# Optimization experiments

Measured on AMD Instinct MI355X. Metric: run time of the kernel, lower is better.

Reference implementation:

```python
import jax, jax.numpy as jnp
import numpy as np

B, N, H, M = 1, 1024, 64, 32


def _posenc(n, d):
    # sinusoidal positional encoding, matches torch PositionalEncoding (eval mode, no dropout)
    pos = jnp.arange(n, dtype=jnp.float32)[:, None]
    div = jnp.exp(jnp.arange(0, d, 2, dtype=jnp.float32) * (-np.log(10000.0) / d))
    ang = pos * div  # [n, d//2]
    pe = jnp.zeros((n, d), jnp.float32)
    pe = pe.at[:, 0::2].set(jnp.sin(ang))
    pe = pe.at[:, 1::2].set(jnp.cos(ang))
    return pe


def _egnn(x, h, m2f, w_msg, b_msg, w_pos, b_pos, w_feat, b_feat):
    # x: [B,N,3], h: [B,N,Hd], m2f: [B,N,N] float pair mask (diag zero)
    Bn, Nn, Hd = h.shape
    m2 = m2f[..., None]
    # r[b,i,j] = x[b,j] - x[b,i]  (torch: x.unsqueeze(-3) - x.unsqueeze(-2))
    r = (x[:, None, :, :] - x[:, :, None, :]) * m2  # [B,N,N,3]
    d2 = jnp.sum(r * r, axis=-1)  # [B,N,N]
    # message_mlp(cat(hi, hj, d2)): hi[b,i,j]=h[j], hj[b,i,j]=h[i]
    # split weight to avoid materializing the N x N x (2H+1) concat
    Wa, Wb, wd = w_msg[:, :Hd], w_msg[:, Hd:2 * Hd], w_msg[:, 2 * Hd]
    A = h @ Wa.T   # [B,N,M], contribution of h_j (hi slot)
    Bm = h @ Wb.T  # [B,N,M], contribution of h_i (hj slot)
    m = jax.nn.relu(A[:, None, :, :] + Bm[:, :, None, :] + d2[..., None] * wd + b_msg) * m2  # [B,N,N,M]
    mx = (m @ w_pos.T + b_pos) * r  # [B,N,N,3]
    x = x + jnp.sum(mx, axis=-2) / (Nn - 1)
    msum = jnp.sum(m, axis=-2)  # [B,N,M]
    h = jnp.concatenate([h, msum], axis=-1) @ w_feat.T + b_feat  # [B,N,Hd]
    return x, h


def setup_inputs() -> dict:
    key = jax.random.key(0)
    ks = jax.random.split(key, 16)
    def lin_w(k, o, i):
        return (jax.random.normal(k, (o, i), jnp.float32) / np.sqrt(i)).astype(jnp.float32)
    def lin_b(k, o):
        return (jax.random.normal(k, (o,), jnp.float32) * 0.02).astype(jnp.float32)
    return {
        'positions': jax.random.normal(ks[0], (B, N, 3), jnp.float32),
        'features': jax.random.normal(ks[1], (B, N, H), jnp.float32),
        'mask': jnp.ones((B, N), dtype=bool),
        'w_msg1': lin_w(ks[2], M, 2 * H + 1), 'b_msg1': lin_b(ks[3], M),
        'w_pos1': lin_w(ks[4], 3, M), 'b_pos1': lin_b(ks[5], 3),
        'w_feat1': lin_w(ks[6], H, M + H), 'b_feat1': lin_b(ks[7], H),
        'w_msg2': lin_w(ks[8], M, 2 * H + 1), 'b_msg2': lin_b(ks[9], M),
        'w_pos2': lin_w(ks[10], 3, M), 'b_pos2': lin_b(ks[11], 3),
        'w_feat2': lin_w(ks[12], H, M + H), 'b_feat2': lin_b(ks[13], H),
        't': 0,
    }


def reference(positions, features, mask,
              w_msg1, b_msg1, w_pos1, b_pos1, w_feat1, b_feat1,
              w_msg2, b_msg2, w_pos2, b_pos2, w_feat2, b_feat2, t):
    Bn, Nn, Hd = features.shape
    h = features + _posenc(Nn, Hd)[None]
    mask2 = mask[:, None, :] & mask[:, :, None]
    mask2 = mask2 & (~jnp.eye(Nn, dtype=bool))[None]  # zero self-pairs
    m2f = mask2.astype(positions.dtype)
    x = positions
    x, h = _egnn(x, h, m2f, w_msg1, b_msg1, w_pos1, b_pos1, w_feat1, b_feat1)
    h = jax.nn.relu(h)
    x, h = _egnn(x, h, m2f, w_msg2, b_msg2, w_pos2, b_pos2, w_feat2, b_feat2)
    return x
```

## Files before the change

kernel.cpp:

```cpp
#include <hip/hip_runtime.h>

#define N    1024
#define HD   64
#define MD   32
#define BLK  256
#define BLKP 512
#define WROW (2 * HD + 1)

typedef _Float16 h2 __attribute__((ext_vector_type(2)));

__device__ __forceinline__ float dot2(h2 a, h2 b, float c)
{
#if __has_builtin(__builtin_amdgcn_fdot2)
    return __builtin_amdgcn_fdot2(a, b, c, false);
#else
    return c + (float)a[0] * (float)b[0] + (float)a[1] * (float)b[1];
#endif
}
__device__ __forceinline__ h2 pack2(float x, float y)
{
    h2 r; r[0] = (_Float16)x; r[1] = (_Float16)y; return r;
}

__global__ __launch_bounds__(BLK) void k_p0(const float* __restrict__ feat,
                                            const float* __restrict__ wmsg,
                                            const float* __restrict__ bmsg,
                                            float* __restrict__ h0,
                                            float* __restrict__ A,
                                            float* __restrict__ Bb,
                                            _Float16* __restrict__ Ah)
{
    __shared__ float scr[4160 + 4 * HD];
    const int tid = threadIdx.x;
    const int n0  = blockIdx.x * 4;

    for (int u = tid; u < MD * WROW; u += BLK) scr[u] = wmsg[u];
    float* hrow = scr + 4160;
    {
        const int n = n0 + (tid >> 6), d = tid & 63;
        const float div = expf((float)(d & ~1) * (-9.210340371976184f / 64.0f));
        const float ang = (float)n * div;
        const float pe  = (d & 1) ? cosf(ang) : sinf(ang);
        const float hv  = feat[n * HD + d] + pe;
        h0[n * HD + d] = hv;
        hrow[tid] = hv;
    }
    __syncthreads();
    if (tid < 4 * MD) {
        const int nl = tid >> 5, m = tid & 31;
        const float* wa = scr + m * WROW;
        const float* hr = hrow + nl * HD;
        float sa = 0.f, sb = bmsg[m];
#pragma unroll
        for (int c = 0; c < HD; c++) {
            const float hv = hr[c];
            sa = fmaf(hv, wa[c], sa);
            sb = fmaf(hv, wa[HD + c], sb);
        }
        const int n = n0 + nl;
        A[n * MD + m]  = sa;
        Bb[n * MD + m] = sb;
        Ah[n * MD + m] = (_Float16)sa;
    }
}

template<int LAYER1>
__global__ __launch_bounds__(BLKP) void k_pair(
    const float* __restrict__ xsrc, const float* __restrict__ Aap,
    const _Float16* __restrict__ Ahp, const float* __restrict__ Bbp,
    const float* __restrict__ wmsg, const float* __restrict__ wpos,
    const float* __restrict__ bpos, float* __restrict__ xout,
    const float* __restrict__ h0, const float* __restrict__ wf,
    const float* __restrict__ bf, const float* __restrict__ wmsg2,
    const float* __restrict__ bmsg2, float* __restrict__ A2,
    float* __restrict__ B2, _Float16* __restrict__ A2h)
{
    const int tid   = threadIdx.x;
    const int wid   = tid >> 6;
    const int lane  = tid & 63;
    const int jslot = lane & 7;
    const int kq    = lane >> 3;

    __shared__ float4 rd[2 * N];
    __shared__ float  wacc[8][8];
    __shared__ float  msAl[8][MD];
    __shared__ float  msBl[8][MD];
    __shared__ float  SxL[3];
    __shared__ float  msF[2][MD];
    __shared__ float  h0r[2][HD];
    __shared__ float  h1r[2][HD];
    float4* rdA = rd;
    float4* rdB = rd + N;

    const int iA = blockIdx.x, iB = blockIdx.x + N / 2;
    const float xiA0 = xsrc[iA * 3 + 0], xiA1 = xsrc[iA * 3 + 1], xiA2 = xsrc[iA * 3 + 2];
    const float xiB0 = xsrc[iB * 3 + 0], xiB1 = xsrc[iB * 3 + 1], xiB2 = xsrc[iB * 3 + 2];

    float sx0 = 0.f, sx1 = 0.f, sx2 = 0.f;
#pragma unroll
    for (int q = 0; q < N / BLKP; q++) {
        const int j = q * BLKP + tid;
        const float xj0 = xsrc[j * 3 + 0];
        const float xj1 = xsrc[j * 3 + 1];
        const float xj2 = xsrc[j * 3 + 2];
        sx0 += xj0; sx1 += xj1; sx2 += xj2;
        float r0 = xj0 - xiA0, r1 = xj1 - xiA1, r2 = xj2 - xiA2;
        float d2 = fmaf(r0, r0, fmaf(r1, r1, r2 * r2));
        rdA[j] = make_float4(r0, r1, r2, __builtin_bit_cast(float, pack2(d2, d2)));
        r0 = xj0 - xiB0; r1 = xj1 - xiB1; r2 = xj2 - xiB2;
        d2 = fmaf(r0, r0, fmaf(r1, r1, r2 * r2));
        rdB[j] = make_float4(r0, r1, r2, __builtin_bit_cast(float, pack2(d2, d2)));
    }
#pragma unroll
    for (int off = 32; off > 0; off >>= 1) {
        sx0 += __shfl_xor(sx0, off);
        sx1 += __shfl_xor(sx1, off);
        sx2 += __shfl_xor(sx2, off);
    }
    if (lane == 0) { wacc[wid][0] = sx0; wacc[wid][1] = sx1; wacc[wid][2] = sx2; }
    __syncthreads();
    if (tid == 0) {
        float s0 = 0.f, s1 = 0.f, s2 = 0.f;
#pragma unroll
        for (int w = 0; w < 8; w++) { s0 += wacc[w][0]; s1 += wacc[w][1]; s2 += wacc[w][2]; }
        SxL[0] = s0; SxL[1] = s1; SxL[2] = s2;
    }

    const float4 biA4 = *(const float4*)(Bbp + iA * MD + kq * 4);
    const float4 biB4 = *(const float4*)(Bbp + iB * MD + kq * 4);
    const float4 wpx4 = *(const float4*)(wpos + kq * 4);
    const float4 wpy4 = *(const float4*)(wpos + MD + kq * 4);
    const float4 wpz4 = *(const float4*)(wpos + 2 * MD + kq * 4);
    const h2 biA01 = pack2(biA4.x, biA4.y), biA23 = pack2(biA4.z, biA4.w);
    const h2 biB01 = pack2(biB4.x, biB4.y), biB23 = pack2(biB4.z, biB4.w);
    const h2 wpx01 = pack2(wpx4.x, wpx4.y), wpx23 = pack2(wpx4.z, wpx4.w);
    const h2 wpy01 = pack2(wpy4.x, wpy4.y), wpy23 = pack2(wpy4.z, wpy4.w);
    const h2 wpz01 = pack2(wpz4.x, wpz4.y), wpz23 = pack2(wpz4.z, wpz4.w);
    const h2 wd01 = pack2(wmsg[(kq * 4 + 0) * WROW + 2 * HD],
                          wmsg[(kq * 4 + 1) * WROW + 2 * HD]);
    const h2 wd23 = pack2(wmsg[(kq * 4 + 2) * WROW + 2 * HD],
                          wmsg[(kq * 4 + 3) * WROW + 2 * HD]);
    const h2 hz = pack2(0.f, 0.f);

    float aA0 = 0.f, aA1 = 0.f, aA2 = 0.f, aB0 = 0.f, aB1 = 0.f, aB2 = 0.f;
    h2 msA01 = hz, msA23 = hz, msB01 = hz, msB23 = hz;

    const int jb = wid * (N / 8);
#pragma unroll 8
    for (int it = 0; it < N / 8 / 8; it++) {
        const int j = jb + it * 8 + jslot;
        const uint2 au = *(const uint2*)(Ahp + j * MD + kq * 4);
        const h2 a01 = __builtin_bit_cast(h2, au.x);
        const h2 a23 = __builtin_bit_cast(h2, au.y);
        const float4 fA = rdA[j];
        const float4 fB = rdB[j];
        const h2 d2A = __builtin_bit_cast(h2, fA.w);
        const h2 d2B = __builtin_bit_cast(h2, fB.w);

        const h2 mA01 = __builtin_elementwise_max(d2A * wd01 + (a01 + biA01), hz);
        const h2 mA23 = __builtin_elementwise_max(d2A * wd23 + (a23 + biA23), hz);
        const h2 mB01 = __builtin_elementwise_max(d2B * wd01 + (a01 + biB01), hz);
        const h2 mB23 = __builtin_elementwise_max(d2B * wd23 + (a23 + biB23), hz);
        if (LAYER1) { msA01 += mA01; msA23 += mA23; msB01 += mB01; msB23 += mB23; }

        const float sAx = dot2(mA23, wpx23, dot2(mA01, wpx01, 0.f));
        const float sAy = dot2(mA23, wpy23, dot2(mA01, wpy01, 0.f));
        const float sAz = dot2(mA23, wpz23, dot2(mA01, wpz01, 0.f));
        const float sBx = dot2(mB23, wpx23, dot2(mB01, wpx01, 0.f));
        const float sBy = dot2(mB23, wpy23, dot2(mB01, wpy01, 0.f));
        const float sBz = dot2(mB23, wpz23, dot2(mB01, wpz01, 0.f));
        aA0 = fmaf(sAx, fA.x, aA0);
        aA1 = fmaf(sAy, fA.y, aA1);
        aA2 = fmaf(sAz, fA.z, aA2);
        aB0 = fmaf(sBx, fB.x, aB0);
        aB1 = fmaf(sBy, fB.y, aB1);
        aB2 = fmaf(sBz, fB.z, aB2);
    }

#pragma unroll
    for (int off = 32; off > 0; off >>= 1) {
        aA0 += __shfl_xor(aA0, off); aA1 += __shfl_xor(aA1, off); aA2 += __shfl_xor(aA2, off);
        aB0 += __shfl_xor(aB0, off); aB1 += __shfl_xor(aB1, off); aB2 += __shfl_xor(aB2, off);
    }
    float msAf[4], msBf[4];
    if (LAYER1) {
        msAf[0] = (float)msA01[0]; msAf[1] = (float)msA01[1];
        msAf[2] = (float)msA23[0]; msAf[3] = (float)msA23[1];
        msBf[0] = (float)msB01[0]; msBf[1] = (float)msB01[1];
        msBf[2] = (float)msB23[0]; msBf[3] = (float)msB23[1];
#pragma unroll
        for (int off = 1; off <= 4; off <<= 1) {
#pragma unroll
            for (int kk = 0; kk < 4; kk++) {
                msAf[kk] += __shfl_xor(msAf[kk], off);
                msBf[kk] += __shfl_xor(msBf[kk], off);
            }
        }
    }
    __syncthreads();
    if (lane == 0) {
        wacc[wid][0] = aA0; wacc[wid][1] = aA1; wacc[wid][2] = aA2;
        wacc[wid][3] = aB0; wacc[wid][4] = aB1; wacc[wid][5] = aB2;
    }
    if (LAYER1 && jslot == 0) {
#pragma unroll
        for (int kk = 0; kk < 4; kk++) {
            msAl[wid][kq * 4 + kk] = msAf[kk];
            msBl[wid][kq * 4 + kk] = msBf[kk];
        }
    }
    __syncthreads();

    if (tid == 0) {
        const float bp0 = bpos[0], bp1 = bpos[1], bp2 = bpos[2];
        float vA0 = 0.f, vA1 = 0.f, vA2 = 0.f, vB0 = 0.f, vB1 = 0.f, vB2 = 0.f;
#pragma unroll
        for (int w = 0; w < 8; w++) {
            vA0 += wacc[w][0]; vA1 += wacc[w][1]; vA2 += wacc[w][2];
            vB0 += wacc[w][3]; vB1 += wacc[w][4]; vB2 += wacc[w][5];
        }
        const float inv = 1.0f / 1023.0f;
        xout[iA * 3 + 0] = xiA0 + (vA0 + bp0 * (SxL[0] - (float)N * xiA0)) * inv;
        xout[iA * 3 + 1] = xiA1 + (vA1 + bp1 * (SxL[1] - (float)N * xiA1)) * inv;
        xout[iA * 3 + 2] = xiA2 + (vA2 + bp2 * (SxL[2] - (float)N * xiA2)) * inv;
        xout[iB * 3 + 0] = xiB0 + (vB0 + bp0 * (SxL[0] - (float)N * xiB0)) * inv;
        xout[iB * 3 + 1] = xiB1 + (vB1 + bp1 * (SxL[1] - (float)N * xiB1)) * inv;
        xout[iB * 3 + 2] = xiB2 + (vB2 + bp2 * (SxL[2] - (float)N * xiB2)) * inv;
    }

    if (LAYER1) {
        float* scr = (float*)rd;
        if (tid < 2 * MD) {
            const int row = tid >> 5, k = tid & 31;
            const int i = row ? iB : iA;
            const float (*ml)[MD] = row ? msBl : msAl;
            float s = 0.f;
#pragma unroll
            for (int w = 0; w < 8; w++) s += ml[w][k];
            s -= fmaxf(Aap[i * MD + k] + Bbp[i * MD + k], 0.f);
            msF[row][k] = s;
        }
        for (int u = tid; u < HD * (HD + MD); u += BLKP) {
            const int o = u / (HD + MD), c = u - o * (HD + MD);
            scr[o * 97 + c] = wf[u];
        }
        if (tid < 2 * HD) {
            const int row = tid >> 6, d = tid & 63;
            h0r[row][d] = h0[(row ? iB : iA) * HD + d];
        }
        __syncthreads();
        if (tid < 2 * HD) {
            const int row = tid >> 6, o = tid & 63;
            const float* w = scr + o * 97;
            float s = bf[o];
#pragma unroll
            for (int c = 0; c < HD; c++) s = fmaf(h0r[row][c], w[c], s);
#pragma unroll
            for (int k = 0; k < MD; k++) s = fmaf(msF[row][k], w[HD + k], s);
            h1r[row][o] = fmaxf(s, 0.f);
        }
        __syncthreads();
        for (int u = tid; u < MD * WROW; u += BLKP) scr[u] = wmsg2[u];
        __syncthreads();
        if (tid < 2 * MD) {
            const int row = tid >> 5, m = tid & 31;
            const float* wa = scr + m * WROW;
            const float* hr = h1r[row];
            float sa = 0.f, sb = bmsg2[m];
#pragma unroll
            for (int c = 0; c < HD; c++) {
                const float hv = hr[c];
                sa = fmaf(hv, wa[c], sa);
                sb = fmaf(hv, wa[HD + c], sb);
            }
            const int i = row ? iB : iA;
            A2[i * MD + m]  = sa;
            B2[i * MD + m]  = sb;
            A2h[i * MD + m] = (_Float16)sa;
        }
    }
}

extern "C" void kernel_launch(void* const* d_in, const int* in_sizes, int n_in,
                              void* d_out, int out_size, void* d_ws, size_t ws_size,
                              hipStream_t stream)
{
    const float* pos     = (const float*)d_in[0];
    const float* feat    = (const float*)d_in[1];
    const float* w_msg1  = (const float*)d_in[3];
    const float* b_msg1  = (const float*)d_in[4];
    const float* w_pos1  = (const float*)d_in[5];
    const float* b_pos1  = (const float*)d_in[6];
    const float* w_feat1 = (const float*)d_in[7];
    const float* b_feat1 = (const float*)d_in[8];
    const float* w_msg2  = (const float*)d_in[9];
    const float* b_msg2  = (const float*)d_in[10];
    const float* w_pos2  = (const float*)d_in[11];
    const float* b_pos2  = (const float*)d_in[12];

    float* ws  = (float*)d_ws;
    float* h0  = ws;
    float* A1  = h0  + N * HD;
    float* B1  = A1  + N * MD;
    float* x1  = B1  + N * MD;
    float* A2  = x1  + N * 4;
    float* B2  = A2  + N * MD;
    _Float16* Ah1 = (_Float16*)(B2 + N * MD);
    _Float16* Ah2 = Ah1 + N * MD;

    k_p0<<<N / 4, BLK, 0, stream>>>(feat, w_msg1, b_msg1, h0, A1, B1, Ah1);
    k_pair<1><<<N / 2, BLKP, 0, stream>>>(pos, A1, Ah1, B1, w_msg1, w_pos1, b_pos1, x1,
                                          h0, w_feat1, b_feat1, w_msg2, b_msg2,
                                          A2, B2, Ah2);
    k_pair<0><<<N / 2, BLKP, 0, stream>>>(x1, A2, Ah2, B2, w_msg2, w_pos2, b_pos2,
                                          (float*)d_out,
                                          nullptr, nullptr, nullptr, nullptr,
                                          nullptr, nullptr, nullptr, nullptr);
}
```

Baseline: 36.00 us.

## Share one pair buffer per j and widen lanes to eight message channels

Stores a single float4 per j holding the A-row displacement and packed half d2 for both rows, and derives the B-row displacement by adding the constant xi difference. This halves the shared memory used for pair data. Each lane now handles 8 message channels, loaded with 16-byte loads, and 16 j-slots per wave, which reduces shared reads and makes longer dot-product chains. The message-sum reduction is reworked to match the new lane mapping. Computing the B displacement by addition may change rounding slightly, and each lane now needs more registers.

```diff
diff --git a/kernel.cpp b/kernel.cpp
--- a/kernel.cpp
+++ b/kernel.cpp
@@ -78,10 +78,10 @@
     const int tid   = threadIdx.x;
     const int wid   = tid >> 6;
     const int lane  = tid & 63;
-    const int jslot = lane & 7;
-    const int kq    = lane >> 3;
-
-    __shared__ float4 rd[2 * N];
+    const int kq    = lane & 3;
+    const int jslot = lane >> 2;
+
+    __shared__ float  sbuf[6848];
     __shared__ float  wacc[8][8];
     __shared__ float  msAl[8][MD];
     __shared__ float  msBl[8][MD];
@@ -89,12 +89,12 @@
     __shared__ float  msF[2][MD];
     __shared__ float  h0r[2][HD];
     __shared__ float  h1r[2][HD];
-    float4* rdA = rd;
-    float4* rdB = rd + N;
+    float4* rd = (float4*)sbuf;
 
     const int iA = blockIdx.x, iB = blockIdx.x + N / 2;
     const float xiA0 = xsrc[iA * 3 + 0], xiA1 = xsrc[iA * 3 + 1], xiA2 = xsrc[iA * 3 + 2];
     const float xiB0 = xsrc[iB * 3 + 0], xiB1 = xsrc[iB * 3 + 1], xiB2 = xsrc[iB * 3 + 2];
+    const float dx0 = xiA0 - xiB0, dx1 = xiA1 - xiB1, dx2 = xiA2 - xiB2;
 
     float sx0 = 0.f, sx1 = 0.f, sx2 = 0.f;
 #pragma unroll
@@ -104,12 +104,11 @@
         const float xj1 = xsrc[j * 3 + 1];
         const float xj2 = xsrc[j * 3 + 2];
         sx0 += xj0; sx1 += xj1; sx2 += xj2;
-        float r0 = xj0 - xiA0, r1 = xj1 - xiA1, r2 = xj2 - xiA2;
-        float d2 = fmaf(r0, r0, fmaf(r1, r1, r2 * r2));
-        rdA[j] = make_float4(r0, r1, r2, __builtin_bit_cast(float, pack2(d2, d2)));
-        r0 = xj0 - xiB0; r1 = xj1 - xiB1; r2 = xj2 - xiB2;
-        d2 = fmaf(r0, r0, fmaf(r1, r1, r2 * r2));
-        rdB[j] = make_float4(r0, r1, r2, __builtin_bit_cast(float, pack2(d2, d2)));
+        const float a0 = xj0 - xiA0, a1 = xj1 - xiA1, a2 = xj2 - xiA2;
+        const float d2A = fmaf(a0, a0, fmaf(a1, a1, a2 * a2));
+        const float b0 = xj0 - xiB0, b1 = xj1 - xiB1, b2 = xj2 - xiB2;
+        const float d2B = fmaf(b0, b0, fmaf(b1, b1, b2 * b2));
+        rd[j] = make_float4(a0, a1, a2, __builtin_bit_cast(float, pack2(d2A, d2B)));
     }
 #pragma unroll
     for (int off = 32; off > 0; off >>= 1) {
@@ -126,55 +125,71 @@
         SxL[0] = s0; SxL[1] = s1; SxL[2] = s2;
     }
 
-    const float4 biA4 = *(const float4*)(Bbp + iA * MD + kq * 4);
-    const float4 biB4 = *(const float4*)(Bbp + iB * MD + kq * 4);
-    const float4 wpx4 = *(const float4*)(wpos + kq * 4);
-    const float4 wpy4 = *(const float4*)(wpos + MD + kq * 4);
-    const float4 wpz4 = *(const float4*)(wpos + 2 * MD + kq * 4);
-    const h2 biA01 = pack2(biA4.x, biA4.y), biA23 = pack2(biA4.z, biA4.w);
-    const h2 biB01 = pack2(biB4.x, biB4.y), biB23 = pack2(biB4.z, biB4.w);
-    const h2 wpx01 = pack2(wpx4.x, wpx4.y), wpx23 = pack2(wpx4.z, wpx4.w);
-    const h2 wpy01 = pack2(wpy4.x, wpy4.y), wpy23 = pack2(wpy4.z, wpy4.w);
-    const h2 wpz01 = pack2(wpz4.x, wpz4.y), wpz23 = pack2(wpz4.z, wpz4.w);
-    const h2 wd01 = pack2(wmsg[(kq * 4 + 0) * WROW + 2 * HD],
-                          wmsg[(kq * 4 + 1) * WROW + 2 * HD]);
-    const h2 wd23 = pack2(wmsg[(kq * 4 + 2) * WROW + 2 * HD],
-                          wmsg[(kq * 4 + 3) * WROW + 2 * HD]);
+    h2 biA[4], biB[4], wpx[4], wpy[4], wpz[4], wd[4];
+    {
+        const float4 bA0 = *(const float4*)(Bbp + iA * MD + kq * 8);
+        const float4 bA1 = *(const float4*)(Bbp + iA * MD + kq * 8 + 4);
+        const float4 bB0 = *(const float4*)(Bbp + iB * MD + kq * 8);
+        const float4 bB1 = *(const float4*)(Bbp + iB * MD + kq * 8 + 4);
+        biA[0] = pack2(bA0.x, bA0.y); biA[1] = pack2(bA0.z, bA0.w);
+        biA[2] = pack2(bA1.x, bA1.y); biA[3] = pack2(bA1.z, bA1.w);
+        biB[0] = pack2(bB0.x, bB0.y); biB[1] = pack2(bB0.z, bB0.w);
+        biB[2] = pack2(bB1.x, bB1.y); biB[3] = pack2(bB1.z, bB1.w);
+        const float4 px0 = *(const float4*)(wpos + kq * 8);
+        const float4 px1 = *(const float4*)(wpos + kq * 8 + 4);
+        const float4 py0 = *(const float4*)(wpos + MD + kq * 8);
+        const float4 py1 = *(const float4*)(wpos + MD + kq * 8 + 4);
+        const float4 pz0 = *(const float4*)(wpos + 2 * MD + kq * 8);
+        const float4 pz1 = *(const float4*)(wpos + 2 * MD + kq * 8 + 4);
+        wpx[0] = pack2(px0.x, px0.y); wpx[1] = pack2(px0.z, px0.w);
+        wpx[2] = pack2(px1.x, px1.y); wpx[3] = pack2(px1.z, px1.w);
+        wpy[0] = pack2(py0.x, py0.y); wpy[1] = pack2(py0.z, py0.w);
+        wpy[2] = pack2(py1.x, py1.y); wpy[3] = pack2(py1.z, py1.w);
+        wpz[0] = pack2(pz0.x, pz0.y); wpz[1] = pack2(pz0.z, pz0.w);
+        wpz[2] = pack2(pz1.x, pz1.y); wpz[3] = pack2(pz1.z, pz1.w);
+#pragma unroll
+        for (int t = 0; t < 4; t++)
+            wd[t] = pack2(wmsg[(kq * 8 + 2 * t) * WROW + 2 * HD],
+                          wmsg[(kq * 8 + 2 * t + 1) * WROW + 2 * HD]);
+    }
     const h2 hz = pack2(0.f, 0.f);
 
     float aA0 = 0.f, aA1 = 0.f, aA2 = 0.f, aB0 = 0.f, aB1 = 0.f, aB2 = 0.f;
-    h2 msA01 = hz, msA23 = hz, msB01 = hz, msB23 = hz;
+    h2 msA[4] = {hz, hz, hz, hz}, msB[4] = {hz, hz, hz, hz};
 
     const int jb = wid * (N / 8);
 #pragma unroll 8
-    for (int it = 0; it < N / 8 / 8; it++) {
-        const int j = jb + it * 8 + jslot;
-        const uint2 au = *(const uint2*)(Ahp + j * MD + kq * 4);
-        const h2 a01 = __builtin_bit_cast(h2, au.x);
-        const h2 a23 = __builtin_bit_cast(h2, au.y);
-        const float4 fA = rdA[j];
-        const float4 fB = rdB[j];
-        const h2 d2A = __builtin_bit_cast(h2, fA.w);
-        const h2 d2B = __builtin_bit_cast(h2, fB.w);
-
-        const h2 mA01 = __builtin_elementwise_max(d2A * wd01 + (a01 + biA01), hz);
-        const h2 mA23 = __builtin_elementwise_max(d2A * wd23 + (a23 + biA23), hz);
-        const h2 mB01 = __builtin_elementwise_max(d2B * wd01 + (a01 + biB01), hz);
-        const h2 mB23 = __builtin_elementwise_max(d2B * wd23 + (a23 + biB23), hz);
-        if (LAYER1) { msA01 += mA01; msA23 += mA23; msB01 += mB01; msB23 += mB23; }
-
-        const float sAx = dot2(mA23, wpx23, dot2(mA01, wpx01, 0.f));
-        const float sAy = dot2(mA23, wpy23, dot2(mA01, wpy01, 0.f));
-        const float sAz = dot2(mA23, wpz23, dot2(mA01, wpz01, 0.f));
-        const float sBx = dot2(mB23, wpx23, dot2(mB01, wpx01, 0.f));
-        const float sBy = dot2(mB23, wpy23, dot2(mB01, wpy01, 0.f));
-        const float sBz = dot2(mB23, wpz23, dot2(mB01, wpz01, 0.f));
-        aA0 = fmaf(sAx, fA.x, aA0);
-        aA1 = fmaf(sAy, fA.y, aA1);
-        aA2 = fmaf(sAz, fA.z, aA2);
-        aB0 = fmaf(sBx, fB.x, aB0);
-        aB1 = fmaf(sBy, fB.y, aB1);
-        aB2 = fmaf(sBz, fB.z, aB2);
+    for (int it = 0; it < 8; it++) {
+        const int j = jb + it * 16 + jslot;
+        const uint4 au = *(const uint4*)(Ahp + j * MD + kq * 8);
+        h2 a[4];
+        a[0] = __builtin_bit_cast(h2, au.x); a[1] = __builtin_bit_cast(h2, au.y);
+        a[2] = __builtin_bit_cast(h2, au.z); a[3] = __builtin_bit_cast(h2, au.w);
+        const float4 f = rd[j];
+        const h2 dd = __builtin_bit_cast(h2, f.w);
+        const h2 dA = __builtin_shufflevector(dd, dd, 0, 0);
+        const h2 dB = __builtin_shufflevector(dd, dd, 1, 1);
+        const float rB0 = f.x + dx0, rB1 = f.y + dx1, rB2 = f.z + dx2;
+
+        h2 mA[4], mB[4];
+#pragma unroll
+        for (int t = 0; t < 4; t++) {
+            mA[t] = __builtin_elementwise_max(dA * wd[t] + (a[t] + biA[t]), hz);
+            mB[t] = __builtin_elementwise_max(dB * wd[t] + (a[t] + biB[t]), hz);
+            if (LAYER1) { msA[t] += mA[t]; msB[t] += mB[t]; }
+        }
+        const float sAx = dot2(mA[3], wpx[3], dot2(mA[2], wpx[2], dot2(mA[1], wpx[1], dot2(mA[0], wpx[0], 0.f))));
+        const float sAy = dot2(mA[3], wpy[3], dot2(mA[2], wpy[2], dot2(mA[1], wpy[1], dot2(mA[0], wpy[0], 0.f))));
+        const float sAz = dot2(mA[3], wpz[3], dot2(mA[2], wpz[2], dot2(mA[1], wpz[1], dot2(mA[0], wpz[0], 0.f))));
+        const float sBx = dot2(mB[3], wpx[3], dot2(mB[2], wpx[2], dot2(mB[1], wpx[1], dot2(mB[0], wpx[0], 0.f))));
+        const float sBy = dot2(mB[3], wpy[3], dot2(mB[2], wpy[2], dot2(mB[1], wpy[1], dot2(mB[0], wpy[0], 0.f))));
+        const float sBz = dot2(mB[3], wpz[3], dot2(mB[2], wpz[2], dot2(mB[1], wpz[1], dot2(mB[0], wpz[0], 0.f))));
+        aA0 = fmaf(sAx, f.x, aA0);
+        aA1 = fmaf(sAy, f.y, aA1);
+        aA2 = fmaf(sAz, f.z, aA2);
+        aB0 = fmaf(sBx, rB0, aB0);
+        aB1 = fmaf(sBy, rB1, aB1);
+        aB2 = fmaf(sBz, rB2, aB2);
     }
 
 #pragma unroll
@@ -182,18 +197,19 @@
         aA0 += __shfl_xor(aA0, off); aA1 += __shfl_xor(aA1, off); aA2 += __shfl_xor(aA2, off);
         aB0 += __shfl_xor(aB0, off); aB1 += __shfl_xor(aB1, off); aB2 += __shfl_xor(aB2, off);
     }
-    float msAf[4], msBf[4];
+    float msAf[8], msBf[8];
     if (LAYER1) {
-        msAf[0] = (float)msA01[0]; msAf[1] = (float)msA01[1];
-        msAf[2] = (float)msA23[0]; msAf[3] = (float)msA23[1];
-        msBf[0] = (float)msB01[0]; msBf[1] = (float)msB01[1];
-        msBf[2] = (float)msB23[0]; msBf[3] = (float)msB23[1];
-#pragma unroll
-        for (int off = 1; off <= 4; off <<= 1) {
-#pragma unroll
-            for (int kk = 0; kk < 4; kk++) {
-                msAf[kk] += __shfl_xor(msAf[kk], off);
-                msBf[kk] += __shfl_xor(msBf[kk], off);
+#pragma unroll
+        for (int t = 0; t < 4; t++) {
+            msAf[2 * t] = (float)msA[t][0]; msAf[2 * t + 1] = (float)msA[t][1];
+            msBf[2 * t] = (float)msB[t][0]; msBf[2 * t + 1] = (float)msB[t][1];
+        }
+#pragma unroll
+        for (int off = 4; off <= 32; off <<= 1) {
+#pragma unroll
+            for (int t = 0; t < 8; t++) {
+                msAf[t] += __shfl_xor(msAf[t], off);
+                msBf[t] += __shfl_xor(msBf[t], off);
             }
         }
     }
@@ -204,9 +220,9 @@
     }
     if (LAYER1 && jslot == 0) {
 #pragma unroll
-        for (int kk = 0; kk < 4; kk++) {
-            msAl[wid][kq * 4 + kk] = msAf[kk];
-            msBl[wid][kq * 4 + kk] = msBf[kk];
+        for (int t = 0; t < 8; t++) {
+            msAl[wid][kq * 8 + t] = msAf[t];
+            msBl[wid][kq * 8 + t] = msBf[t];
         }
     }
     __syncthreads();
@@ -229,7 +245,7 @@
     }
 
     if (LAYER1) {
-        float* scr = (float*)rd;
+        float* scr = sbuf;
         if (tid < 2 * MD) {
             const int row = tid >> 5, k = tid & 31;
             const int i = row ? iB : iA;
```

Measured after the change: 33.68 us (median of 2 runs). 1.07x faster.
